# Kernel tuning notes

Measured on AMD Instinct MI355X. Metric: run time of the kernel, lower is better.

The kernel has to match this reference:

```python
import jax, jax.numpy as jnp
import numpy as np

D_MODEL = 2048
N_HEADS = 16
HEAD_DIM = D_MODEL // N_HEADS
B, T = 4, 2048


def setup_inputs() -> dict:
    key = jax.random.key(0)
    ks = jax.random.split(key, 10)
    s = 1.0 / np.sqrt(D_MODEL)
    x = jax.random.normal(ks[0], (B, T, D_MODEL), dtype=jnp.float32)
    # causal additive mask, broadcastable to [B, H, T, T]
    neg = jnp.finfo(jnp.float32).min
    causal = jnp.triu(jnp.full((T, T), neg, dtype=jnp.float32), k=1)
    mask = causal[None, None, :, :]
    return {
        "x": x,
        "mask": mask,
        "Wq": jax.random.uniform(ks[1], (D_MODEL, D_MODEL), jnp.float32, -s, s),
        "bq": jax.random.uniform(ks[2], (D_MODEL,), jnp.float32, -s, s),
        "Wk": jax.random.uniform(ks[3], (D_MODEL, HEAD_DIM), jnp.float32, -s, s),
        "bk": jax.random.uniform(ks[4], (HEAD_DIM,), jnp.float32, -s, s),
        "Wv": jax.random.uniform(ks[5], (D_MODEL, HEAD_DIM), jnp.float32, -s, s),
        "bv": jax.random.uniform(ks[6], (HEAD_DIM,), jnp.float32, -s, s),
        "Wo": jax.random.uniform(ks[7], (D_MODEL, D_MODEL), jnp.float32, -s, s),
        "bo": jax.random.uniform(ks[8], (D_MODEL,), jnp.float32, -s, s),
    }


def reference(x, mask, Wq, bq, Wk, bk, Wv, bv, Wo, bo):
    Bb, Tt, _ = x.shape
    H, Dh = N_HEADS, HEAD_DIM
    scale = 1.0 / jnp.sqrt(jnp.float32(Dh))
    q = (x @ Wq + bq).reshape(Bb, Tt, H, Dh)          # [B,T,H,D]
    k = x @ Wk + bk                                    # [B,T,D] (single KV head)
    v = x @ Wv + bv                                    # [B,T,D]
    # scores: [B,H,T,T] — q heads against shared k
    attn = jnp.einsum("bthd,bsd->bhts", q, k) * scale
    attn = attn + mask
    attn = jax.nn.softmax(attn, axis=-1)
    out = jnp.einsum("bhts,bsd->bthd", attn, v).reshape(Bb, Tt, D_MODEL)
    return out @ Wo + bo
```

## Files before the change

kernel.cpp:

```cpp
#include <hip/hip_runtime.h>
#include <hip/hip_bf16.h>
#include <stdint.h>

#define DEV __device__ __forceinline__

typedef unsigned short u16;
typedef unsigned int u32;
typedef __bf16 bf16x8 __attribute__((ext_vector_type(8)));
typedef float f32x4 __attribute__((ext_vector_type(4)));
typedef u16 u16x4 __attribute__((ext_vector_type(4)));
typedef u32 u32x4 __attribute__((ext_vector_type(4)));

typedef __attribute__((address_space(1))) u32 u32_as1;
typedef __attribute__((address_space(3))) u32 u32_as3;

static constexpr int Bn = 4, Tn = 2048, Dm = 2048, Hn = 16, Dh = 128;
static constexpr int BT = Bn * Tn;
static constexpr int KVSTR = 256;
static constexpr float CL2 = 0.1275174147f;

#define VMCNT(n) asm volatile("s_waitcnt vmcnt(" #n ")" ::: "memory")
#define BARRIER() __builtin_amdgcn_s_barrier()

DEV u16 f2bf(float f) {
  u32 u = __builtin_bit_cast(u32, f);
  u += 0x7fffu + ((u >> 16) & 1u);
  return (u16)(u >> 16);
}
DEV u16 cvt_bf(float f) { return __builtin_bit_cast(u16, (__bf16)f); }
DEV u32 cvt_pk_bf16(float lo, float hi) {
  u32 r;
  asm("v_cvt_pk_bf16_f32 %0, %1, %2" : "=v"(r) : "v"(lo), "v"(hi));
  return r;
}

DEV void gl2lds16(const void* g, void* l) {
  __builtin_amdgcn_global_load_lds((u32_as1*)(uintptr_t)g,
                                   (u32_as3*)(u32)(uintptr_t)l, 16, 0, 0);
}

__global__ __launch_bounds__(256) void k_prep(const float* __restrict__ x,
                                              u16* __restrict__ xb,
                                              const float* __restrict__ Wq,
                                              u16* __restrict__ Wqt,
                                              const float* __restrict__ Wo,
                                              u16* __restrict__ Wot,
                                              const float* __restrict__ Wk,
                                              const float* __restrict__ Wv,
                                              u16* __restrict__ Wkvt) {
  const int z = blockIdx.z;
  const int xx = threadIdx.x, yy = threadIdx.y;
  if (z == 0) {
    const int tid = yy * 32 + xx;
    int i = (blockIdx.y * 64 + blockIdx.x) * 1024 + tid;
#pragma unroll
    for (int k = 0; k < 4; ++k, i += 256) {
      f32x4 v = ((const f32x4*)x)[i];
      u16x4 o;
      o.x = f2bf(v.x); o.y = f2bf(v.y); o.z = f2bf(v.z); o.w = f2bf(v.w);
      ((u16x4*)xb)[i] = o;
    }
    return;
  }
  const float* in; u16* out; int R, C;
  if (z == 1)      { in = Wq; out = Wqt; R = Dm; C = Dm; }
  else if (z == 2) { in = Wo; out = Wot; R = Dm; C = Dm; }
  else if (z == 3) { in = Wk; out = Wkvt; R = Dm; C = Dh; }
  else             { in = Wv; out = Wkvt + (size_t)Dh * Dm; R = Dm; C = Dh; }
  if (blockIdx.x * 32 >= C) return;
  __shared__ float t[32][33];
  const int r0 = blockIdx.y * 32, c0 = blockIdx.x * 32;
#pragma unroll
  for (int i = 0; i < 4; ++i)
    t[yy + i * 8][xx] = in[(size_t)(r0 + yy + i * 8) * C + c0 + xx];
  __syncthreads();
#pragma unroll
  for (int i = 0; i < 4; ++i)
    out[(size_t)(c0 + yy + i * 8) * R + r0 + xx] = f2bf(t[xx][yy + i * 8]);
}

__global__ __launch_bounds__(256) void k_transpose_v(const u16* __restrict__ in,
                                                     int inStride,
                                                     u16* __restrict__ out,
                                                     int R, int C) {
  __shared__ u16 t[32][34];
  const int r0 = blockIdx.y * 32, c0 = blockIdx.x * 32;
  const int x = threadIdx.x, y = threadIdx.y;
#pragma unroll
  for (int i = 0; i < 4; ++i)
    t[y + i * 8][x] = in[(size_t)(r0 + y + i * 8) * inStride + c0 + x];
  __syncthreads();
  const int sx = (((x & 7) >> 2) << 4) | (((x >> 3) & 3) << 2) | (x & 3);
#pragma unroll
  for (int i = 0; i < 4; ++i)
    out[(size_t)(c0 + y + i * 8) * R + r0 + x] = t[sx][y + i * 8];
}

__global__ __launch_bounds__(256) void k_gemm_kv(const u16* __restrict__ A,
                                                 const u16* __restrict__ Bt,
                                                 float* __restrict__ P,
                                                 int M, int N, int K) {
  __shared__ __align__(128) char smem[32768];
  char* As = smem;
  char* Bs = smem + 16384;
  const int tid = threadIdx.x;
  const int wid = tid >> 6, lane = tid & 63;
  const int g = lane >> 4, r = lane & 15;
  const int wr = wid >> 1, wc = wid & 1;
  const int m0 = blockIdx.x * 128, n0 = blockIdx.y * 128;
  const int kbase = blockIdx.z * 512;
  P += (size_t)blockIdx.z * M * N;

  f32x4 acc[4][4];
#pragma unroll
  for (int m = 0; m < 4; ++m)
#pragma unroll
    for (int n = 0; n < 4; ++n) acc[m][n] = (f32x4)(0.f);

  for (int k0 = kbase; k0 < kbase + 512; k0 += 64) {
#pragma unroll
    for (int n = 0; n < 4; ++n) {
      const int L = n * 4096 + tid * 16;
      const int row = L >> 7;
      const int colb = (L & 127) ^ ((row & 7) << 4);
      gl2lds16((const char*)A + ((size_t)(m0 + row) * K + k0) * 2 + colb, As + L);
      gl2lds16((const char*)Bt + ((size_t)(n0 + row) * K + k0) * 2 + colb, Bs + L);
    }
    __syncthreads();
#pragma unroll
    for (int kk = 0; kk < 2; ++kk) {
      bf16x8 a[4], b[4];
#pragma unroll
      for (int m = 0; m < 4; ++m) {
        const int row = wr * 64 + m * 16 + r;
        a[m] = *(const bf16x8*)(As + row * 128 + ((kk * 64 + g * 16) ^ ((row & 7) << 4)));
      }
#pragma unroll
      for (int n = 0; n < 4; ++n) {
        const int row = wc * 64 + n * 16 + r;
        b[n] = *(const bf16x8*)(Bs + row * 128 + ((kk * 64 + g * 16) ^ ((row & 7) << 4)));
      }
#pragma unroll
      for (int m = 0; m < 4; ++m)
#pragma unroll
        for (int n = 0; n < 4; ++n)
          acc[m][n] = __builtin_amdgcn_mfma_f32_16x16x32_bf16(a[m], b[n], acc[m][n], 0, 0, 0);
    }
    __syncthreads();
  }

#pragma unroll
  for (int n = 0; n < 4; ++n) {
    const int col = n0 + wc * 64 + n * 16 + r;
#pragma unroll
    for (int m = 0; m < 4; ++m)
#pragma unroll
      for (int j = 0; j < 4; ++j) {
        const int grow = m0 + wr * 64 + m * 16 + 4 * g + j;
        P[(size_t)grow * N + col] = acc[m][n][j];
      }
  }
}

__global__ __launch_bounds__(256) void k_kv_reduce(const float* __restrict__ P,
                                                   const float* __restrict__ bk,
                                                   const float* __restrict__ bv,
                                                   u16* __restrict__ KV) {
  const int i = blockIdx.x * 256 + threadIdx.x;
  const size_t S = (size_t)BT * KVSTR / 4;
  f32x4 s0 = ((const f32x4*)P)[i];
  f32x4 s1 = ((const f32x4*)P)[i + S];
  f32x4 s2 = ((const f32x4*)P)[i + 2 * S];
  f32x4 s3 = ((const f32x4*)P)[i + 3 * S];
  const int col = (i * 4) & (KVSTR - 1);
  u16x4 o;
#pragma unroll
  for (int j = 0; j < 4; ++j) {
    const int c = col + j;
    const float b = (c < Dh) ? bk[c] : bv[c - Dh];
    o[j] = cvt_bf((s0[j] + s1[j]) + (s2[j] + s3[j]) + b);
  }
  ((u16x4*)KV)[i] = o;
}

template <typename OutT>
__global__ __launch_bounds__(512, 2) void k_gemm256(const u16* __restrict__ A,
                                                    const u16* __restrict__ Bt,
                                                    const float* __restrict__ bias,
                                                    OutT* __restrict__ C,
                                                    int M, int N, int K,
                                                    float oscale) {
  extern __shared__ char smem[];
  const int tid = threadIdx.x;
  const int wid = tid >> 6, lane = tid & 63;
  const int g = lane >> 4, r = lane & 15;
  const int wm = wid >> 2, wn = wid & 3;

  const int nbn = N >> 8;
  const int cpx = gridDim.x >> 3;
  const int linear = (blockIdx.x & 7) * cpx + (blockIdx.x >> 3);
  const int m0 = (linear / nbn) << 8;
  const int n0 = (linear % nbn) << 8;

  const bool aEarly = (wid & 3) < 2;
  const bool bEarly = (wid & 1) == 0;

  const int rowInCh = lane >> 3;
  const int colb = ((lane & 7) << 4) ^ (rowInCh << 4);
  const char* srcA0; const char* srcA1; const char* srcA2; const char* srcA3;
  const char* srcB0; const char* srcB1; const char* srcB2; const char* srcB3;
  int ldsA[4], ldsB[4];
  {
    const int wnh = (wid >> 1) & 1;
    const int cbb = ((wid >> 2) << 1) | (wid & 1);
    const char* sa[4]; const char* sb[4];
#pragma unroll
    for (int i = 0; i < 4; ++i) {
      const int chA = ((wid & 3) << 2) + i;
      const int lrA = (wm << 7) + (chA << 3) + rowInCh;
      sa[i] = (const char*)A + ((size_t)(m0 + lrA) * K) * 2 + colb;
      ldsA[i] = ((wm << 7) + (chA << 3)) * 128 + lane * 16;
      const int chB = (cbb << 2) + i;
      const int lrB = (wnh << 7) + (chB << 3) + rowInCh;
      sb[i] = (const char*)Bt + ((size_t)(n0 + lrB) * K) * 2 + colb;
      ldsB[i] = 32768 + ((wnh << 7) + (chB << 3)) * 128 + lane * 16;
    }
    srcA0 = sa[0]; srcA1 = sa[1]; srcA2 = sa[2]; srcA3 = sa[3];
    srcB0 = sb[0]; srcB1 = sb[1]; srcB2 = sb[2]; srcB3 = sb[3];
  }

  auto stageA = [&](int t, int b) {
    const size_t ko = (size_t)t * 128;
    char* base = smem + (b << 16);
    gl2lds16(srcA0 + ko, base + ldsA[0]);
    gl2lds16(srcA1 + ko, base + ldsA[1]);
    gl2lds16(srcA2 + ko, base + ldsA[2]);
    gl2lds16(srcA3 + ko, base + ldsA[3]);
  };
  auto stageB = [&](int t, int b) {
    const size_t ko = (size_t)t * 128;
    char* base = smem + (b << 16);
    gl2lds16(srcB0 + ko, base + ldsB[0]);
    gl2lds16(srcB1 + ko, base + ldsB[1]);
    gl2lds16(srcB2 + ko, base + ldsB[2]);
    gl2lds16(srcB3 + ko, base + ldsB[3]);
  };

  f32x4 acc[8][4];
#pragma unroll
  for (int m = 0; m < 8; ++m)
#pragma unroll
    for (int n = 0; n < 4; ++n) acc[m][n] = (f32x4)(0.f);

  auto readA = [&](const char* Ab, int qm, bf16x8 (&a)[8]) {
#pragma unroll
    for (int m = 0; m < 4; ++m) {
      const int row = (wm << 7) + ((qm * 4 + m) << 4) + r;
#pragma unroll
      for (int kk = 0; kk < 2; ++kk)
        a[m * 2 + kk] = *(const bf16x8*)(Ab + row * 128 + ((kk * 64 + g * 16) ^ ((row & 7) << 4)));
    }
  };
  auto readB = [&](const char* Bb, int qn, bf16x8 (&b)[4]) {
#pragma unroll
    for (int n = 0; n < 2; ++n) {
      const int row = (wn << 6) + ((qn * 2 + n) << 4) + r;
#pragma unroll
      for (int kk = 0; kk < 2; ++kk)
        b[n * 2 + kk] = *(const bf16x8*)(Bb + row * 128 + ((kk * 64 + g * 16) ^ ((row & 7) << 4)));
    }
  };
  auto mfmaQ = [&](const bf16x8 (&a)[8], const bf16x8 (&b)[4], int qm, int qn) {
    __builtin_amdgcn_s_setprio(1);
#pragma unroll
    for (int m = 0; m < 4; ++m)
#pragma unroll
      for (int n = 0; n < 2; ++n)
#pragma unroll
        for (int kk = 0; kk < 2; ++kk)
          acc[qm * 4 + m][qn * 2 + n] = __builtin_amdgcn_mfma_f32_16x16x32_bf16(
              a[m * 2 + kk], b[n * 2 + kk], acc[qm * 4 + m][qn * 2 + n], 0, 0, 0);
    __builtin_amdgcn_s_setprio(0);
  };

  const int NT = K >> 6;
  stageA(0, 0); stageB(0, 0);
  stageA(1, 1); stageB(1, 1);
  VMCNT(8);
  BARRIER();

  bf16x8 a0[8], a1[8], b0[4], b1[4];
  for (int t = 0; t < NT; ++t) {
    const char* Ab = smem + ((t & 1) << 16);
    const char* Bb = Ab + 32768;
    const bool pre = (t + 2 < NT);
    readA(Ab, 0, a0);
    readB(Bb, 0, b0);
    BARRIER();
    if (pre) {
      if (aEarly) stageA(t + 2, t & 1);
      if (bEarly) stageB(t + 2, t & 1);
    }
    mfmaQ(a0, b0, 0, 0);
    BARRIER();
    readB(Bb, 1, b1);
    BARRIER();
    if (pre && !bEarly) stageB(t + 2, t & 1);
    mfmaQ(a0, b1, 0, 1);
    BARRIER();
    readA(Ab, 1, a1);
    BARRIER();
    if (pre && !aEarly) stageA(t + 2, t & 1);
    mfmaQ(a1, b1, 1, 1);
    BARRIER();
    mfmaQ(a1, b0, 1, 0);
    if (pre) { VMCNT(8); } else { VMCNT(0); }
    BARRIER();
  }

#pragma unroll
  for (int n = 0; n < 4; ++n) {
    const int col = n0 + wn * 64 + n * 16 + r;
    const float bv = bias[col];
#pragma unroll
    for (int m = 0; m < 8; ++m) {
#pragma unroll
      for (int j = 0; j < 4; ++j) {
        const int grow = m0 + wm * 128 + m * 16 + 4 * g + j;
        const float v = (acc[m][n][j] + bv) * oscale;
        if constexpr (sizeof(OutT) == 2)
          ((u16*)C)[(size_t)grow * N + col] = cvt_bf(v);
        else
          ((float*)C)[(size_t)grow * N + col] = v;
      }
    }
  }
}

__global__ __launch_bounds__(256, 2) void k_attn(const u16* __restrict__ Q,
                                                 const u16* __restrict__ Kb,
                                                 const u16* __restrict__ VT,
                                                 u16* __restrict__ O) {
  __shared__ __align__(1024) char smem[65536];

  const int tid = threadIdx.x;
  const int wq = tid >> 6, lane = tid & 63;
  const int g = lane >> 4, r = lane & 15;

  const int bid = blockIdx.x;
  const int xcd = bid & 7, ii = bid >> 3;
  const int b = xcd >> 1;
  const int h = ((xcd & 1) << 3) | (ii >> 3);
  const int p = ii & 7;
  const int qtA = p, qtB = 15 - p;
  const int nstA = 2 * qtA + 2;
  const int ntot = nstA + 2 * qtB + 2;

  const float FM = 16.0f;

  bf16x8 qf[2][4];
  f32x4 o[2][8];
  float lrow[2];

  auto loadQ = [&](int qrow0) {
#pragma unroll
    for (int m2 = 0; m2 < 2; ++m2)
#pragma unroll
      for (int c = 0; c < 4; ++c)
        qf[m2][c] = *(const bf16x8*)(Q + (size_t)(qrow0 + m2 * 16 + r) * Dm + h * Dh + c * 32 + g * 8);
  };
  auto resetAcc = [&]() {
#pragma unroll
    for (int m2 = 0; m2 < 2; ++m2) {
#pragma unroll
      for (int c = 0; c < 8; ++c) o[m2][c] = (f32x4)(0.f);
      lrow[m2] = 0.f;
    }
  };
  auto storeO = [&](int qrow0) {
#pragma unroll
    for (int m2 = 0; m2 < 2; ++m2) {
      float lt = lrow[m2];
      lt += __shfl_xor(lt, 16);
      lt += __shfl_xor(lt, 32);
      float linv[4];
#pragma unroll
      for (int j = 0; j < 4; ++j)
        linv[j] = __builtin_amdgcn_rcpf(__shfl(lt, 20 * g + j));
#pragma unroll
      for (int c = 0; c < 8; ++c)
#pragma unroll
        for (int j = 0; j < 4; ++j)
          O[(size_t)(qrow0 + m2 * 16 + 4 * g + j) * Dm + h * Dh + c * 16 + r] =
              cvt_bf(o[m2][c][j] * linv[j]);
    }
  };
  auto stageK = [&](int s0, char* dst) {
#pragma unroll
    for (int n = 0; n < 4; ++n) {
      const int L = n * 4096 + tid * 16;
      const int row = L >> 8;
      const int colb = (L & 255) ^ ((row & 7) << 4);
      gl2lds16((const char*)Kb + (size_t)(s0 + row) * (KVSTR * 2) + colb, dst + L);
    }
  };
  auto stageV = [&](int s0, char* dst) {
#pragma unroll
    for (int n = 0; n < 4; ++n) {
      const int L = n * 4096 + tid * 16;
      const int row = L >> 7;
      const int colb = (L & 127) ^ ((row & 7) << 4);
      gl2lds16((const char*)VT + ((size_t)row * BT + s0) * 2 + colb, dst + L);
    }
  };

  int qt = qtA;
  int qrow0 = b * Tn + qt * 128 + wq * 32;
  int qmin = qt * 128 + wq * 32;
  loadQ(qrow0);
  resetAcc();
  stageK(b * Tn, smem);
  stageV(b * Tn, smem + 32768);

  int cur = 0;
  for (int t = 0; t < ntot; ++t) {
    VMCNT(0);
    BARRIER();

    if (t == nstA) {
      storeO(qrow0);
      qt = qtB;
      qrow0 = b * Tn + qt * 128 + wq * 32;
      qmin = qt * 128 + wq * 32;
      loadQ(qrow0);
      resetAcc();
    }
    const int st = (t < nstA) ? t : t - nstA;

    {
      const int t1 = t + 1;
      const int st1 = (t1 >= ntot) ? 0 : ((t1 < nstA) ? t1 : t1 - nstA);
      stageK(b * Tn + st1 * 64, smem + ((cur ^ 1) << 14));
      stageV(b * Tn + st1 * 64, smem + 32768 + ((cur ^ 1) << 14));
    }

    const bool fullmask = (st * 64 >= qmin + 32);
    if (!fullmask) {
      const char* Kc = smem + (cur << 14);
      const char* Vb = smem + 32768 + (cur << 14);
      f32x4 sf[2][4];
      __builtin_amdgcn_s_setprio(1);
#pragma unroll
      for (int n = 0; n < 4; ++n) {
        f32x4 sa = (f32x4)(0.f), sb = (f32x4)(0.f);
#pragma unroll
        for (int c = 0; c < 4; ++c) {
          const int row = n * 16 + r;
          bf16x8 kf = *(const bf16x8*)(Kc + row * 256 + ((c * 64 + g * 16) ^ ((row & 7) << 4)));
          sa = __builtin_amdgcn_mfma_f32_16x16x32_bf16(kf, qf[0][c], sa, 0, 0, 0);
          sb = __builtin_amdgcn_mfma_f32_16x16x32_bf16(kf, qf[1][c], sb, 0, 0, 0);
        }
        sf[0][n] = sa; sf[1][n] = sb;
      }
      __builtin_amdgcn_s_setprio(0);
      if (st * 64 + 63 > qmin) {
#pragma unroll
        for (int m2 = 0; m2 < 2; ++m2) {
          const int q = qmin + m2 * 16 + r;
#pragma unroll
          for (int n = 0; n < 4; ++n)
#pragma unroll
            for (int j = 0; j < 4; ++j) {
              const int key = st * 64 + n * 16 + 4 * g + j;
              if (key > q) sf[m2][n][j] = -1e30f;
            }
        }
      }
      u32x4 pau[2][2];
#pragma unroll
      for (int m2 = 0; m2 < 2; ++m2) {
#pragma unroll
        for (int n = 0; n < 4; ++n) {
          const float p0 = __builtin_amdgcn_exp2f(sf[m2][n][0] - FM);
          const float p1 = __builtin_amdgcn_exp2f(sf[m2][n][1] - FM);
          const float p2 = __builtin_amdgcn_exp2f(sf[m2][n][2] - FM);
          const float p3 = __builtin_amdgcn_exp2f(sf[m2][n][3] - FM);
          lrow[m2] += (p0 + p1) + (p2 + p3);
          pau[m2][n >> 1][(n & 1) * 2]     = cvt_pk_bf16(p0, p1);
          pau[m2][n >> 1][(n & 1) * 2 + 1] = cvt_pk_bf16(p2, p3);
        }
      }

      __builtin_amdgcn_s_setprio(1);
#pragma unroll
      for (int kk = 0; kk < 2; ++kk) {
        if (st * 64 + kk * 32 >= qmin + 32) continue;
        const bf16x8 pa0 = __builtin_bit_cast(bf16x8, pau[0][kk]);
        const bf16x8 pa1 = __builtin_bit_cast(bf16x8, pau[1][kk]);
#pragma unroll
        for (int c = 0; c < 8; ++c) {
          const int row = c * 16 + r;
          const bf16x8 vb = *(const bf16x8*)(Vb + row * 128 + ((kk * 64 + g * 16) ^ ((row & 7) << 4)));
          o[0][c] = __builtin_amdgcn_mfma_f32_16x16x32_bf16(pa0, vb, o[0][c], 0, 0, 0);
          o[1][c] = __builtin_amdgcn_mfma_f32_16x16x32_bf16(pa1, vb, o[1][c], 0, 0, 0);
        }
      }
      __builtin_amdgcn_s_setprio(0);
    }
    cur ^= 1;
  }
  storeO(qrow0);
}

extern "C" void kernel_launch(void* const* d_in, const int* in_sizes, int n_in,
                              void* d_out, int out_size, void* d_ws, size_t ws_size,
                              hipStream_t stream) {
  const float* x  = (const float*)d_in[0];
  const float* Wq = (const float*)d_in[2];
  const float* bq = (const float*)d_in[3];
  const float* Wk = (const float*)d_in[4];
  const float* bk = (const float*)d_in[5];
  const float* Wv = (const float*)d_in[6];
  const float* bv = (const float*)d_in[7];
  const float* Wo = (const float*)d_in[8];
  const float* bo = (const float*)d_in[9];
  float* out = (float*)d_out;

  char* ws = (char*)d_ws;
  size_t off = 0;
  auto alloc = [&](size_t bytes) {
    char* p = ws + off;
    off += (bytes + 255) & ~(size_t)255;
    return p;
  };
  u16* xb   = (u16*)alloc((size_t)BT * Dm * 2);
  u16* Qb   = (u16*)alloc((size_t)BT * Dm * 2);
  u16* KVb  = (u16*)alloc((size_t)BT * KVSTR * 2);
  u16* VTb  = (u16*)alloc((size_t)BT * Dh * 2);
  u16* Wqt  = (u16*)alloc((size_t)Dm * Dm * 2);
  u16* Wkvt = (u16*)alloc((size_t)Dm * KVSTR * 2);
  u16* Wot  = (u16*)alloc((size_t)Dm * Dm * 2);
  u16* Ob   = xb;
  float* Pkv = (float*)Qb;

  hipFuncSetAttribute(reinterpret_cast<const void*>(&k_gemm256<u16>),
                      hipFuncAttributeMaxDynamicSharedMemorySize, 131072);
  hipFuncSetAttribute(reinterpret_cast<const void*>(&k_gemm256<float>),
                      hipFuncAttributeMaxDynamicSharedMemorySize, 131072);

  dim3 tb(32, 8);
  k_prep<<<dim3(64, 64, 5), tb, 0, stream>>>(x, xb, Wq, Wqt, Wo, Wot, Wk, Wv, Wkvt);

  k_gemm_kv<<<dim3(BT / 128, KVSTR / 128, 4), 256, 0, stream>>>(xb, Wkvt, Pkv, BT, KVSTR, Dm);
  k_kv_reduce<<<BT * KVSTR / 4 / 256, 256, 0, stream>>>(Pkv, bk, bv, KVb);

  k_gemm256<u16><<<(BT / 256) * (Dm / 256), 512, 131072, stream>>>(xb, Wqt, bq, Qb, BT, Dm, Dm, CL2);
  k_transpose_v<<<dim3(Dh / 32, BT / 32), tb, 0, stream>>>(KVb + Dh, KVSTR, VTb, BT, Dh);

  k_attn<<<512, 256, 0, stream>>>(Qb, KVb, VTb, Ob);

  k_gemm256<float><<<(BT / 256) * (Dm / 256), 512, 131072, stream>>>(Ob, Wot, bo, out, BT, Dm, Dm, 1.0f);
}
```

Before: 263.2 us.

## Double-buffer KV GEMM staging and simplify main GEMM pipeline to prefetch-one

The KV split-K GEMM now double-buffers its LDS tiles, issuing the next K-tile's global-to-LDS loads before computing the current one, and raises MFMA priority. The large 256x256 GEMM drops its two-deep prefetch with staggered per-wave staging and many barriers in favour of a single prefetch per iteration with one wait and barrier at the top. This cuts barrier overhead in the main GEMM, but each iteration now waits for all outstanding loads, so less memory latency is hidden than with the deeper pipeline.

```diff
diff --git a/kernel.cpp b/kernel.cpp
--- a/kernel.cpp
+++ b/kernel.cpp
@@ -100,9 +100,7 @@
                                                  const u16* __restrict__ Bt,
                                                  float* __restrict__ P,
                                                  int M, int N, int K) {
-  __shared__ __align__(128) char smem[32768];
-  char* As = smem;
-  char* Bs = smem + 16384;
+  __shared__ __align__(1024) char smem[65536];
   const int tid = threadIdx.x;
   const int wid = tid >> 6, lane = tid & 63;
   const int g = lane >> 4, r = lane & 15;
@@ -111,22 +109,32 @@
   const int kbase = blockIdx.z * 512;
   P += (size_t)blockIdx.z * M * N;
 
-  f32x4 acc[4][4];
-#pragma unroll
-  for (int m = 0; m < 4; ++m)
-#pragma unroll
-    for (int n = 0; n < 4; ++n) acc[m][n] = (f32x4)(0.f);
-
-  for (int k0 = kbase; k0 < kbase + 512; k0 += 64) {
+  auto stage = [&](int tt) {
+    const int k0 = kbase + tt * 64;
+    char* base = smem + ((tt & 1) << 15);
 #pragma unroll
     for (int n = 0; n < 4; ++n) {
       const int L = n * 4096 + tid * 16;
       const int row = L >> 7;
       const int colb = (L & 127) ^ ((row & 7) << 4);
-      gl2lds16((const char*)A + ((size_t)(m0 + row) * K + k0) * 2 + colb, As + L);
-      gl2lds16((const char*)Bt + ((size_t)(n0 + row) * K + k0) * 2 + colb, Bs + L);
-    }
-    __syncthreads();
+      gl2lds16((const char*)A + ((size_t)(m0 + row) * K + k0) * 2 + colb, base + L);
+      gl2lds16((const char*)Bt + ((size_t)(n0 + row) * K + k0) * 2 + colb, base + 16384 + L);
+    }
+  };
+
+  f32x4 acc[4][4];
+#pragma unroll
+  for (int m = 0; m < 4; ++m)
+#pragma unroll
+    for (int n = 0; n < 4; ++n) acc[m][n] = (f32x4)(0.f);
+
+  stage(0);
+  for (int tt = 0; tt < 8; ++tt) {
+    VMCNT(0);
+    BARRIER();
+    const char* As = smem + ((tt & 1) << 15);
+    const char* Bs = As + 16384;
+    if (tt + 1 < 8) stage(tt + 1);
 #pragma unroll
     for (int kk = 0; kk < 2; ++kk) {
       bf16x8 a[4], b[4];
@@ -140,13 +148,14 @@
         const int row = wc * 64 + n * 16 + r;
         b[n] = *(const bf16x8*)(Bs + row * 128 + ((kk * 64 + g * 16) ^ ((row & 7) << 4)));
       }
+      __builtin_amdgcn_s_setprio(1);
 #pragma unroll
       for (int m = 0; m < 4; ++m)
 #pragma unroll
         for (int n = 0; n < 4; ++n)
           acc[m][n] = __builtin_amdgcn_mfma_f32_16x16x32_bf16(a[m], b[n], acc[m][n], 0, 0, 0);
-    }
-    __syncthreads();
+      __builtin_amdgcn_s_setprio(0);
+    }
   }
 
 #pragma unroll
@@ -202,9 +211,6 @@
   const int m0 = (linear / nbn) << 8;
   const int n0 = (linear % nbn) << 8;
 
-  const bool aEarly = (wid & 3) < 2;
-  const bool bEarly = (wid & 1) == 0;
-
   const int rowInCh = lane >> 3;
   const int colb = ((lane & 7) << 4) ^ (rowInCh << 4);
   const char* srcA0; const char* srcA1; const char* srcA2; const char* srcA3;
@@ -229,17 +235,13 @@
     srcB0 = sb[0]; srcB1 = sb[1]; srcB2 = sb[2]; srcB3 = sb[3];
   }
 
-  auto stageA = [&](int t, int b) {
+  auto stage = [&](int t) {
     const size_t ko = (size_t)t * 128;
-    char* base = smem + (b << 16);
+    char* base = smem + ((t & 1) << 16);
     gl2lds16(srcA0 + ko, base + ldsA[0]);
     gl2lds16(srcA1 + ko, base + ldsA[1]);
     gl2lds16(srcA2 + ko, base + ldsA[2]);
     gl2lds16(srcA3 + ko, base + ldsA[3]);
-  };
-  auto stageB = [&](int t, int b) {
-    const size_t ko = (size_t)t * 128;
-    char* base = smem + (b << 16);
     gl2lds16(srcB0 + ko, base + ldsB[0]);
     gl2lds16(srcB1 + ko, base + ldsB[1]);
     gl2lds16(srcB2 + ko, base + ldsB[2]);
@@ -284,38 +286,23 @@
   };
 
   const int NT = K >> 6;
-  stageA(0, 0); stageB(0, 0);
-  stageA(1, 1); stageB(1, 1);
-  VMCNT(8);
-  BARRIER();
+  stage(0);
 
   bf16x8 a0[8], a1[8], b0[4], b1[4];
   for (int t = 0; t < NT; ++t) {
+    VMCNT(0);
+    BARRIER();
     const char* Ab = smem + ((t & 1) << 16);
     const char* Bb = Ab + 32768;
-    const bool pre = (t + 2 < NT);
+    if (t + 1 < NT) stage(t + 1);
     readA(Ab, 0, a0);
     readB(Bb, 0, b0);
-    BARRIER();
-    if (pre) {
-      if (aEarly) stageA(t + 2, t & 1);
-      if (bEarly) stageB(t + 2, t & 1);
-    }
     mfmaQ(a0, b0, 0, 0);
-    BARRIER();
     readB(Bb, 1, b1);
-    BARRIER();
-    if (pre && !bEarly) stageB(t + 2, t & 1);
     mfmaQ(a0, b1, 0, 1);
-    BARRIER();
     readA(Ab, 1, a1);
-    BARRIER();
-    if (pre && !aEarly) stageA(t + 2, t & 1);
     mfmaQ(a1, b1, 1, 1);
-    BARRIER();
     mfmaQ(a1, b0, 1, 0);
-    if (pre) { VMCNT(8); } else { VMCNT(0); }
-    BARRIER();
   }
 
 #pragma unroll
```

After: 267.9 us. Within noise of the previous version (+1.8%).
